# Performance work log

Measured on AMD Instinct MI355X. Metric: run time of the kernel, lower is better.

Reference implementation:

```python
import jax, jax.numpy as jnp
import numpy as np

WEIGHT = 1.0  # init kwarg
B, N, M, D = 32, 128, 128, 256


def _hungarian(cost):
    """O(n^3) Hungarian (Jonker-Volgenant potentials form) on host numpy.
    cost: [n, m] with n <= m. Returns col index assigned to each row
    (row_ind is implicitly arange(n), matching scipy.linear_sum_assignment).
    """
    cost = np.asarray(cost, dtype=np.float64)
    n, m = cost.shape
    u = np.zeros(n + 1)
    v = np.zeros(m + 1)
    p = np.zeros(m + 1, dtype=np.int64)   # p[j] = row (1-based) matched to col j
    way = np.zeros(m + 1, dtype=np.int64)
    for i in range(1, n + 1):
        p[0] = i
        j0 = 0
        minv = np.full(m + 1, np.inf)
        used = np.zeros(m + 1, dtype=bool)
        while True:
            used[j0] = True
            i0 = p[j0]
            free = ~used[1:]
            cur = cost[i0 - 1, :] - u[i0] - v[1:]
            upd = free & (cur < minv[1:])
            minv[1:][upd] = cur[upd]
            way[1:][upd] = j0
            masked = np.where(free, minv[1:], np.inf)
            j1 = int(np.argmin(masked)) + 1
            delta = masked[j1 - 1]
            u[p[used]] += delta
            v[used] -= delta
            minv[1:][free] -= delta
            j0 = j1
            if p[j0] == 0:
                break
        while j0:
            j1 = way[j0]
            p[j0] = p[j1]
            j0 = j1
    col_of_row = np.zeros(n, dtype=np.int64)
    for j in range(1, m + 1):
        if p[j] > 0:
            col_of_row[p[j] - 1] = j - 1
    return col_of_row


def _pairwise_mse(p, g):
    """cost[b,i,j] = mean_d (p[b,i,d]-g[b,j,d])^2, fused without [B,N,M,D] tensor."""
    d = p.shape[-1]
    p2 = jnp.sum(p * p, axis=-1)                    # [B,N]
    g2 = jnp.sum(g * g, axis=-1)                    # [B,M]
    pg = jnp.einsum('bnd,bmd->bnm', p, g)           # [B,N,M]
    return (p2[:, :, None] + g2[:, None, :] - 2.0 * pg) / d


def setup_inputs() -> dict:
    key = jax.random.key(0)
    k1, k2 = jax.random.split(key)
    batch_prediction = jax.random.normal(k1, (B, N, D), dtype=jnp.float32)
    batch_groundtruth = jax.random.normal(k2, (B, M, D), dtype=jnp.float32)
    return {"batch_prediction": batch_prediction,
            "batch_groundtruth": batch_groundtruth}


def reference(batch_prediction, batch_groundtruth):
    b, n = batch_prediction.shape[0], batch_prediction.shape[1]
    cost = _pairwise_mse(batch_prediction, batch_groundtruth)   # [B,N,M]
    cost_np = np.asarray(jax.device_get(cost))
    # Hungarian assignment on host (matches scipy.linear_sum_assignment; CPU-bound)
    cols = jnp.asarray(np.stack([_hungarian(cost_np[bi]) for bi in range(b)]))  # [B,N]
    matched = cost[jnp.arange(b)[:, None], jnp.arange(n)[None, :], cols]        # [B,N]
    loss = matched.mean(axis=1).sum() / b * WEIGHT
    return jnp.reshape(loss, (1,))
```

## Files before the change

### kernel.cpp

```cpp
#include <hip/hip_runtime.h>
#include <hip/hip_fp16.h>
#include <float.h>

#define Bc 32
#define Nn 128
#define Dd 256

#define QSCALE 2048.0f
#define QINV   (1.0f / 2048.0f)
#define GPAD   260

template <int CTRL>
__device__ __forceinline__ float dpp_addsrc(float x) {
    return __int_as_float(__builtin_amdgcn_update_dpp(0, __float_as_int(x), CTRL,
                                                      0xf, 0xf, false));
}
__device__ __forceinline__ float wave_sum_lane63(float x) {
    x += dpp_addsrc<0x121>(x);
    x += dpp_addsrc<0x122>(x);
    x += dpp_addsrc<0x124>(x);
    x += dpp_addsrc<0x128>(x);
    x += dpp_addsrc<0x142>(x);
    x += dpp_addsrc<0x143>(x);
    return x;
}

template <int CTRL>
__device__ __forceinline__ unsigned dpp_movu(unsigned x) {
    return (unsigned)__builtin_amdgcn_update_dpp((int)0xFFFFFFFFu, (int)x, CTRL,
                                                 0xf, 0xf, false);
}
__device__ __forceinline__ unsigned wave_umin_lane63(unsigned x) {
    x = min(x, dpp_movu<0x121>(x));
    x = min(x, dpp_movu<0x122>(x));
    x = min(x, dpp_movu<0x124>(x));
    x = min(x, dpp_movu<0x128>(x));
    x = min(x, dpp_movu<0x142>(x));
    x = min(x, dpp_movu<0x143>(x));
    return x;
}

template <int CTRL>
__device__ __forceinline__ float dpp_movf(float x) {
    return __int_as_float(__builtin_amdgcn_update_dpp(0x7f7fffff, __float_as_int(x),
                                                      CTRL, 0xf, 0xf, false));
}
template <int CTRL>
__device__ __forceinline__ void dpp2min_step(float& m1, float& m2) {
    float o1 = dpp_movf<CTRL>(m1);
    float o2 = dpp_movf<CTRL>(m2);
    float n1 = fminf(m1, o1);
    m2 = fminf(fmaxf(m1, o1), fminf(m2, o2));
    m1 = n1;
}

__device__ __forceinline__ float readlane_f(float v, int lane) {
    return __int_as_float(__builtin_amdgcn_readlane(__float_as_int(v), lane));
}

__global__ __launch_bounds__(256) void matcher_kernel(const float* __restrict__ P,
                                                      const float* __restrict__ G,
                                                      float* __restrict__ ws,
                                                      float* __restrict__ out) {
    const int b = blockIdx.x;
    const int tid = threadIdx.x;
    const int t = tid & 63;
    const int wv = tid >> 6;

    __shared__ float Csh[Nn * Nn];
    __shared__ float gsh[64 * GPAD];
    __shared__ float p2sh[Nn];
    __shared__ int claim[Nn];
    __half2* H = (__half2*)gsh;

    if (tid < Nn) {
        claim[tid] = 0x7fffffff;
        const float4* pr = (const float4*)(P + ((size_t)b * Nn + tid) * Dd);
        float s = 0.f;
        for (int d4 = 0; d4 < Dd / 4; ++d4) {
            float4 v = pr[d4];
            s += v.x * v.x + v.y * v.y + v.z * v.z + v.w * v.w;
        }
        p2sh[tid] = s;
    }

    const float4* G4 = (const float4*)(G + (size_t)b * Nn * Dd);
    for (int h = 0; h < 2; ++h) {
        __syncthreads();
        for (int k = 0; k < 16; ++k) {
            int e = k * 256 + tid;
            int row = e >> 6, c4 = e & 63;
            *(float4*)&gsh[row * GPAD + c4 * 4] = G4[(size_t)(h * 64 + row) * 64 + c4];
        }
        __syncthreads();

        const int jj = t;
        float g2 = 0.f;
        for (int d4 = 0; d4 < 64; ++d4) {
            float4 gv = *(const float4*)&gsh[jj * GPAD + d4 * 4];
            g2 += gv.x * gv.x + gv.y * gv.y + gv.z * gv.z + gv.w * gv.w;
        }
        for (int ii = wv; ii < Nn; ii += 4) {
            const float4* prow = (const float4*)(P + ((size_t)b * Nn + ii) * Dd);
            float pg = 0.f;
#pragma unroll 8
            for (int d4 = 0; d4 < 64; ++d4) {
                float4 pv = prow[d4];
                float4 gv = *(const float4*)&gsh[jj * GPAD + d4 * 4];
                pg += pv.x * gv.x + pv.y * gv.y + pv.z * gv.z + pv.w * gv.w;
            }
            Csh[ii * Nn + h * 64 + jj] =
                (p2sh[ii] + g2 - 2.0f * pg) * (1.0f / (float)Dd);
        }
    }
    __syncthreads();

    for (int e = tid; e < Nn * 64; e += 256) {
        int row = e >> 6, c = e & 63;
        H[e] = __halves2half2(__float2half_rn(Csh[row * Nn + c]),
                              __float2half_rn(Csh[row * Nn + c + 64]));
    }
    __syncthreads();
    if (wv != 0) return;

    float bestA = FLT_MAX, bestB = FLT_MAX;
    int argA = 0, argB = 0;
    for (int i = 0; i < Nn; ++i) {
        __half2 hc = H[i * 64 + t];
        float c0 = __low2float(hc);
        float c1 = __high2float(hc);
        if (c0 < bestA) { bestA = c0; argA = i; }
        if (c1 < bestB) { bestB = c1; argB = i; }
    }
    float vA = bestA, vB = bestB;
    atomicMin(&claim[argA], t);
    atomicMin(&claim[argB], t + 64);

    float uA = 0.0f, uB = 0.0f;
    int pA = 0, pB = 0;
    if (claim[argA] == t)      pA = argA + 1;
    if (claim[argB] == t + 64) pB = argB + 1;

    unsigned long long fmA = __ballot(claim[t] == 0x7fffffff);
    unsigned long long fmB = __ballot(claim[t + 64] == 0x7fffffff);

    for (int pass = 0; pass < 3; ++pass) {
        if (!(fmA | fmB)) break;
        unsigned long long remA = fmA, remB = fmB;
        int guard = 0;
        while ((remA | remB) != 0ull && guard++ < 256) {
            int l, i, slotR;
            if (remA) { l = __ffsll(remA) - 1; remA &= remA - 1; i = l + 1;  slotR = 0;
                        if (!((fmA >> l) & 1)) continue; }
            else      { l = __ffsll(remB) - 1; remB &= remB - 1; i = l + 65; slotR = 1;
                        if (!((fmB >> l) & 1)) continue; }

            __half2 hr = H[(i - 1) * 64 + t];
            float cur0 = __low2float(hr) - vA;
            float cur1 = __high2float(hr) - vB;
            float m1 = fminf(cur0, cur1);
            float m2 = fmaxf(cur0, cur1);
            dpp2min_step<0x121>(m1, m2);
            dpp2min_step<0x122>(m1, m2);
            dpp2min_step<0x124>(m1, m2);
            dpp2min_step<0x128>(m1, m2);
            dpp2min_step<0x142>(m1, m2);
            dpp2min_step<0x143>(m1, m2);
            float s_m1 = readlane_f(m1, 63);
            float s_m2 = readlane_f(m2, 63);

            unsigned long long b0 = __ballot(cur0 == s_m1);
            unsigned long long b1 = __ballot(cur1 == s_m1);
            int j1 = b0 ? __ffsll(b0) : (__ffsll(b1) + 64);
            int lane1 = (j1 - 1) & 63, slot1 = (j1 - 1) >> 6;

            if (t == l) { if (slotR == 0) uA = s_m2; else uB = s_m2; }

            int k0 = __builtin_amdgcn_readlane(slot1 ? pB : pA, lane1);
            bool strict = (s_m1 < s_m2);
            if (!strict && k0 != 0) continue;

            if (t == lane1) {
                if (slot1 == 0) { vA += s_m1 - s_m2; pA = i; }
                else            { vB += s_m1 - s_m2; pB = i; }
            }
            if (slotR == 0) fmA &= ~(1ull << l); else fmB &= ~(1ull << l);
            if (k0 != 0) {
                int kl = (k0 - 1) & 63;
                if (k0 <= 64) { fmA |= 1ull << kl; remA |= 1ull << kl; }
                else          { fmB |= 1ull << kl; remB |= 1ull << kl; }
            }
        }
    }

    for (int slotR = 0; slotR < 2; ++slotR) {
        unsigned long long mask = slotR ? fmB : fmA;
        while (mask) {
            int l = __ffsll(mask) - 1;
            mask &= mask - 1;
            int i = l + 1 + slotR * 64;

            float minvA = FLT_MAX, minvB = FLT_MAX;
            int wayA = -1, wayB = -1;
            bool usedA = false, usedB = false;
            bool rUA = false, rUB = false;
            if (t == l) { if (slotR == 0) rUA = true; else rUB = true; }

            int s_j0 = -1;
            float s_u = readlane_f(slotR ? uB : uA, l);
            int s_j1;

            __half2 hc = H[(i - 1) * 64 + t];

            for (;;) {
                float c0 = __low2float(hc);
                float c1 = __high2float(hc);
                if (!usedA) {
                    float cur = fmaxf(c0 - s_u - vA, 0.0f);
                    if (cur < minvA) { minvA = cur; wayA = s_j0; }
                }
                if (!usedB) {
                    float cur = fmaxf(c1 - s_u - vB, 0.0f);
                    if (cur < minvB) { minvB = cur; wayB = s_j0; }
                }

                unsigned kA = usedA ? 0xFFFFFFFFu
                    : ((((unsigned)(fminf(minvA, 30.0f) * QSCALE)) << 16)
                       | ((unsigned)pA << 8) | (unsigned)t);
                unsigned kB = usedB ? 0xFFFFFFFFu
                    : ((((unsigned)(fminf(minvB, 30.0f) * QSCALE)) << 16)
                       | ((unsigned)pB << 8) | (unsigned)(t + 64));
                unsigned k = wave_umin_lane63(min(kA, kB));
                unsigned s_key = (unsigned)__builtin_amdgcn_readlane((int)k, 63);
                float s_delta = (float)(s_key >> 16) * QINV;
                int s_p = (int)((s_key >> 8) & 0xFFu);
                s_j1 = (int)(s_key & 0xFFu);

                int idx = (s_p > 0 ? s_p : 1) - 1;
                __half2 nhc = H[idx * 64 + t];
                float s_unext = readlane_f((idx >> 6) ? uB : uA, idx & 63);

                if (usedA) { vA -= s_delta; } else { minvA = fmaxf(minvA - s_delta, 0.0f); }
                if (usedB) { vB -= s_delta; } else { minvB = fmaxf(minvB - s_delta, 0.0f); }
                if (rUA) uA += s_delta;
                if (rUB) uB += s_delta;

                if (s_p == 0) break;

                if (t == (s_j1 & 63)) { if ((s_j1 >> 6) == 0) usedA = true; else usedB = true; }
                {
                    int r = s_p - 1;
                    if (t == (r & 63)) { if ((r >> 6) == 0) rUA = true; else rUB = true; }
                }
                s_j0 = s_j1;
                s_u = s_unext;
                hc = nhc;
            }

            int s_j = s_j1;
            while (s_j >= 0) {
                int lane = s_j & 63;
                int slot = s_j >> 6;
                int s_jprev = __builtin_amdgcn_readlane(slot ? wayB : wayA, lane);
                int s_pnew;
                if (s_jprev < 0) {
                    s_pnew = i;
                } else {
                    int lp = s_jprev & 63;
                    int sp = s_jprev >> 6;
                    s_pnew = __builtin_amdgcn_readlane(sp ? pB : pA, lp);
                }
                if (t == lane) {
                    if (slot == 0) pA = s_pnew; else pB = s_pnew;
                }
                s_j = s_jprev;
            }
        }
    }

    float tot = Csh[(pA - 1) * Nn + t] + Csh[(pB - 1) * Nn + t + 64];
    tot = wave_sum_lane63(tot);

    if (t == 63) {
        __hip_atomic_store(&ws[b], tot, __ATOMIC_RELEASE, __HIP_MEMORY_SCOPE_AGENT);
    }

    if (b == 0) {
        float v = 0.f;
        if (t < Bc) {
            do {
                v = __hip_atomic_load(&ws[t], __ATOMIC_ACQUIRE, __HIP_MEMORY_SCOPE_AGENT);
            } while (!(v > 0.0f));
        }
        float x = (t < Bc) ? v : 0.0f;
        x = wave_sum_lane63(x);
        if (t == 63) out[0] = x * (1.0f / ((float)Nn * (float)Bc));
    }
}

extern "C" void kernel_launch(void* const* d_in, const int* in_sizes, int n_in,
                              void* d_out, int out_size, void* d_ws, size_t ws_size,
                              hipStream_t stream) {
    const float* P = (const float*)d_in[0];
    const float* G = (const float*)d_in[1];
    float* out = (float*)d_out;
    float* ws = (float*)d_ws;

    matcher_kernel<<<Bc, 256, 0, stream>>>(P, G, ws, out);
}
```

Measured before the change: 581.9 us.

## Use fp32 cost matrix and lazy dual updates in Hungarian augmentation

Drops the fp16 half2 copy of the cost matrix and reads fp32 costs straight from shared memory. The Dijkstra-style augmentation now keeps absolute distances and applies the potential updates once after each search, instead of updating every lane's minv, u and v on each iteration. This takes per-step ALU work out of the serial single-wave loop. The p2/g2/pg dot products are split into four independent accumulators to expose more ILP. Risks are twice the LDS traffic per row fetch and a change in numerics, since quantized keys are now built from absolute distances clamped at 30.

```diff
diff --git a/kernel.cpp b/kernel.cpp
--- a/kernel.cpp
+++ b/kernel.cpp
@@ -1,5 +1,4 @@
 #include <hip/hip_runtime.h>
-#include <hip/hip_fp16.h>
 #include <float.h>
 
 #define Bc 32
@@ -7,7 +6,6 @@
 #define Dd 256
 
 #define QSCALE 2048.0f
-#define QINV   (1.0f / 2048.0f)
 #define GPAD   260
 
 template <int CTRL>
@@ -58,6 +56,10 @@
     return __int_as_float(__builtin_amdgcn_readlane(__float_as_int(v), lane));
 }
 
+__device__ __forceinline__ float dot4(float4 a, float4 b) {
+    return a.x * b.x + a.y * b.y + a.z * b.z + a.w * b.w;
+}
+
 __global__ __launch_bounds__(256) void matcher_kernel(const float* __restrict__ P,
                                                       const float* __restrict__ G,
                                                       float* __restrict__ ws,
@@ -71,17 +73,20 @@
     __shared__ float gsh[64 * GPAD];
     __shared__ float p2sh[Nn];
     __shared__ int claim[Nn];
-    __half2* H = (__half2*)gsh;
 
     if (tid < Nn) {
         claim[tid] = 0x7fffffff;
         const float4* pr = (const float4*)(P + ((size_t)b * Nn + tid) * Dd);
-        float s = 0.f;
-        for (int d4 = 0; d4 < Dd / 4; ++d4) {
-            float4 v = pr[d4];
-            s += v.x * v.x + v.y * v.y + v.z * v.z + v.w * v.w;
-        }
-        p2sh[tid] = s;
+        float a0 = 0.f, a1 = 0.f, a2 = 0.f, a3 = 0.f;
+#pragma unroll
+        for (int d4 = 0; d4 < 64; d4 += 4) {
+            float4 v0 = pr[d4], v1 = pr[d4 + 1], v2 = pr[d4 + 2], v3 = pr[d4 + 3];
+            a0 += dot4(v0, v0);
+            a1 += dot4(v1, v1);
+            a2 += dot4(v2, v2);
+            a3 += dot4(v3, v3);
+        }
+        p2sh[tid] = (a0 + a1) + (a2 + a3);
     }
 
     const float4* G4 = (const float4*)(G + (size_t)b * Nn * Dd);
@@ -95,30 +100,42 @@
         __syncthreads();
 
         const int jj = t;
-        float g2 = 0.f;
-        for (int d4 = 0; d4 < 64; ++d4) {
-            float4 gv = *(const float4*)&gsh[jj * GPAD + d4 * 4];
-            g2 += gv.x * gv.x + gv.y * gv.y + gv.z * gv.z + gv.w * gv.w;
+        float g2;
+        {
+            float a0 = 0.f, a1 = 0.f, a2 = 0.f, a3 = 0.f;
+#pragma unroll
+            for (int d4 = 0; d4 < 64; d4 += 4) {
+                float4 v0 = *(const float4*)&gsh[jj * GPAD + d4 * 4];
+                float4 v1 = *(const float4*)&gsh[jj * GPAD + (d4 + 1) * 4];
+                float4 v2 = *(const float4*)&gsh[jj * GPAD + (d4 + 2) * 4];
+                float4 v3 = *(const float4*)&gsh[jj * GPAD + (d4 + 3) * 4];
+                a0 += dot4(v0, v0);
+                a1 += dot4(v1, v1);
+                a2 += dot4(v2, v2);
+                a3 += dot4(v3, v3);
+            }
+            g2 = (a0 + a1) + (a2 + a3);
         }
         for (int ii = wv; ii < Nn; ii += 4) {
             const float4* prow = (const float4*)(P + ((size_t)b * Nn + ii) * Dd);
-            float pg = 0.f;
-#pragma unroll 8
-            for (int d4 = 0; d4 < 64; ++d4) {
-                float4 pv = prow[d4];
-                float4 gv = *(const float4*)&gsh[jj * GPAD + d4 * 4];
-                pg += pv.x * gv.x + pv.y * gv.y + pv.z * gv.z + pv.w * gv.w;
-            }
+            float a0 = 0.f, a1 = 0.f, a2 = 0.f, a3 = 0.f;
+#pragma unroll
+            for (int d4 = 0; d4 < 64; d4 += 4) {
+                float4 p0 = prow[d4], p1 = prow[d4 + 1];
+                float4 p2 = prow[d4 + 2], p3 = prow[d4 + 3];
+                float4 q0 = *(const float4*)&gsh[jj * GPAD + d4 * 4];
+                float4 q1 = *(const float4*)&gsh[jj * GPAD + (d4 + 1) * 4];
+                float4 q2 = *(const float4*)&gsh[jj * GPAD + (d4 + 2) * 4];
+                float4 q3 = *(const float4*)&gsh[jj * GPAD + (d4 + 3) * 4];
+                a0 += dot4(p0, q0);
+                a1 += dot4(p1, q1);
+                a2 += dot4(p2, q2);
+                a3 += dot4(p3, q3);
+            }
+            float pg = (a0 + a1) + (a2 + a3);
             Csh[ii * Nn + h * 64 + jj] =
                 (p2sh[ii] + g2 - 2.0f * pg) * (1.0f / (float)Dd);
         }
-    }
-    __syncthreads();
-
-    for (int e = tid; e < Nn * 64; e += 256) {
-        int row = e >> 6, c = e & 63;
-        H[e] = __halves2half2(__float2half_rn(Csh[row * Nn + c]),
-                              __float2half_rn(Csh[row * Nn + c + 64]));
     }
     __syncthreads();
     if (wv != 0) return;
@@ -126,9 +143,8 @@
     float bestA = FLT_MAX, bestB = FLT_MAX;
     int argA = 0, argB = 0;
     for (int i = 0; i < Nn; ++i) {
-        __half2 hc = H[i * 64 + t];
-        float c0 = __low2float(hc);
-        float c1 = __high2float(hc);
+        float c0 = Csh[i * Nn + t];
+        float c1 = Csh[i * Nn + t + 64];
         if (c0 < bestA) { bestA = c0; argA = i; }
         if (c1 < bestB) { bestB = c1; argB = i; }
     }
@@ -155,9 +171,9 @@
             else      { l = __ffsll(remB) - 1; remB &= remB - 1; i = l + 65; slotR = 1;
                         if (!((fmB >> l) & 1)) continue; }
 
-            __half2 hr = H[(i - 1) * 64 + t];
-            float cur0 = __low2float(hr) - vA;
-            float cur1 = __high2float(hr) - vB;
+            const float* crow = &Csh[(i - 1) * Nn];
+            float cur0 = crow[t] - vA;
+            float cur1 = crow[t + 64] - vB;
             float m1 = fminf(cur0, cur1);
             float m2 = fmaxf(cur0, cur1);
             dpp2min_step<0x121>(m1, m2);
@@ -200,62 +216,66 @@
             mask &= mask - 1;
             int i = l + 1 + slotR * 64;
 
-            float minvA = FLT_MAX, minvB = FLT_MAX;
+            float dA = FLT_MAX, dB = FLT_MAX;
             int wayA = -1, wayB = -1;
             bool usedA = false, usedB = false;
-            bool rUA = false, rUB = false;
-            if (t == l) { if (slotR == 0) rUA = true; else rUB = true; }
 
             int s_j0 = -1;
+            float s_mu = 0.0f;
             float s_u = readlane_f(slotR ? uB : uA, l);
             int s_j1;
 
-            __half2 hc = H[(i - 1) * 64 + t];
+            float c0 = Csh[(i - 1) * Nn + t];
+            float c1 = Csh[(i - 1) * Nn + t + 64];
 
             for (;;) {
-                float c0 = __low2float(hc);
-                float c1 = __high2float(hc);
+                float s_base = s_mu - s_u;
                 if (!usedA) {
-                    float cur = fmaxf(c0 - s_u - vA, 0.0f);
-                    if (cur < minvA) { minvA = cur; wayA = s_j0; }
+                    float cur = fmaxf(c0 - vA + s_base, 0.0f);
+                    if (cur < dA) { dA = cur; wayA = s_j0; }
                 }
                 if (!usedB) {
-                    float cur = fmaxf(c1 - s_u - vB, 0.0f);
-                    if (cur < minvB) { minvB = cur; wayB = s_j0; }
+                    float cur = fmaxf(c1 - vB + s_base, 0.0f);
+                    if (cur < dB) { dB = cur; wayB = s_j0; }
                 }
 
                 unsigned kA = usedA ? 0xFFFFFFFFu
-                    : ((((unsigned)(fminf(minvA, 30.0f) * QSCALE)) << 16)
+                    : ((((unsigned)(fminf(dA, 30.0f) * QSCALE)) << 16)
                        | ((unsigned)pA << 8) | (unsigned)t);
                 unsigned kB = usedB ? 0xFFFFFFFFu
-                    : ((((unsigned)(fminf(minvB, 30.0f) * QSCALE)) << 16)
+                    : ((((unsigned)(fminf(dB, 30.0f) * QSCALE)) << 16)
                        | ((unsigned)pB << 8) | (unsigned)(t + 64));
                 unsigned k = wave_umin_lane63(min(kA, kB));
                 unsigned s_key = (unsigned)__builtin_amdgcn_readlane((int)k, 63);
-                float s_delta = (float)(s_key >> 16) * QINV;
                 int s_p = (int)((s_key >> 8) & 0xFFu);
                 s_j1 = (int)(s_key & 0xFFu);
 
                 int idx = (s_p > 0 ? s_p : 1) - 1;
-                __half2 nhc = H[idx * 64 + t];
+                float nc0 = Csh[idx * Nn + t];
+                float nc1 = Csh[idx * Nn + t + 64];
                 float s_unext = readlane_f((idx >> 6) ? uB : uA, idx & 63);
-
-                if (usedA) { vA -= s_delta; } else { minvA = fmaxf(minvA - s_delta, 0.0f); }
-                if (usedB) { vB -= s_delta; } else { minvB = fmaxf(minvB - s_delta, 0.0f); }
-                if (rUA) uA += s_delta;
-                if (rUB) uB += s_delta;
+                s_mu = readlane_f((s_j1 >> 6) ? dB : dA, s_j1 & 63);
 
                 if (s_p == 0) break;
 
                 if (t == (s_j1 & 63)) { if ((s_j1 >> 6) == 0) usedA = true; else usedB = true; }
-                {
-                    int r = s_p - 1;
-                    if (t == (r & 63)) { if ((r >> 6) == 0) rUA = true; else rUB = true; }
-                }
                 s_j0 = s_j1;
                 s_u = s_unext;
-                hc = nhc;
-            }
+                c0 = nc0;
+                c1 = nc1;
+            }
+
+            float mustar = s_mu;
+            {
+                int r = i - 1;
+                if (t == (r & 63)) { if ((r >> 6) == 0) uA += mustar; else uB += mustar; }
+            }
+            p2sh[t] = 0.0f;
+            p2sh[t + 64] = 0.0f;
+            if (usedA) { float adj = mustar - dA; vA -= adj; p2sh[pA - 1] = adj; }
+            if (usedB) { float adj = mustar - dB; vB -= adj; p2sh[pB - 1] = adj; }
+            uA += p2sh[t];
+            uB += p2sh[t + 64];
 
             int s_j = s_j1;
             while (s_j >= 0) {
```

Measured after the change: 723.8 us. 24.4% more time.

## Use fp32 cost matrix directly and double block to 512 threads

Applied to the files above, without the earlier changes.

Removes the fp16 half2 packed copy of the cost matrix and has the single-wave Hungarian solver read fp32 costs straight from shared memory. The pairwise-MSE phase is spread over 512 threads (8 waves) instead of 256. This drops one conversion pass and a barrier, and avoids fp16 rounding in the assignment. In exchange, each solver step now does two LDS loads per lane instead of one, and those loads sit on the serial critical path.

```diff
diff --git a/kernel.cpp b/kernel.cpp
--- a/kernel.cpp
+++ b/kernel.cpp
@@ -1,5 +1,4 @@
 #include <hip/hip_runtime.h>
-#include <hip/hip_fp16.h>
 #include <float.h>
 
 #define Bc 32
@@ -58,7 +57,7 @@
     return __int_as_float(__builtin_amdgcn_readlane(__float_as_int(v), lane));
 }
 
-__global__ __launch_bounds__(256) void matcher_kernel(const float* __restrict__ P,
+__global__ __launch_bounds__(512) void matcher_kernel(const float* __restrict__ P,
                                                       const float* __restrict__ G,
                                                       float* __restrict__ ws,
                                                       float* __restrict__ out) {
@@ -71,7 +70,6 @@
     __shared__ float gsh[64 * GPAD];
     __shared__ float p2sh[Nn];
     __shared__ int claim[Nn];
-    __half2* H = (__half2*)gsh;
 
     if (tid < Nn) {
         claim[tid] = 0x7fffffff;
@@ -87,8 +85,8 @@
     const float4* G4 = (const float4*)(G + (size_t)b * Nn * Dd);
     for (int h = 0; h < 2; ++h) {
         __syncthreads();
-        for (int k = 0; k < 16; ++k) {
-            int e = k * 256 + tid;
+        for (int k = 0; k < 8; ++k) {
+            int e = k * 512 + tid;
             int row = e >> 6, c4 = e & 63;
             *(float4*)&gsh[row * GPAD + c4 * 4] = G4[(size_t)(h * 64 + row) * 64 + c4];
         }
@@ -100,7 +98,7 @@
             float4 gv = *(const float4*)&gsh[jj * GPAD + d4 * 4];
             g2 += gv.x * gv.x + gv.y * gv.y + gv.z * gv.z + gv.w * gv.w;
         }
-        for (int ii = wv; ii < Nn; ii += 4) {
+        for (int ii = wv; ii < Nn; ii += 8) {
             const float4* prow = (const float4*)(P + ((size_t)b * Nn + ii) * Dd);
             float pg = 0.f;
 #pragma unroll 8
@@ -114,21 +112,13 @@
         }
     }
     __syncthreads();
-
-    for (int e = tid; e < Nn * 64; e += 256) {
-        int row = e >> 6, c = e & 63;
-        H[e] = __halves2half2(__float2half_rn(Csh[row * Nn + c]),
-                              __float2half_rn(Csh[row * Nn + c + 64]));
-    }
-    __syncthreads();
     if (wv != 0) return;
 
     float bestA = FLT_MAX, bestB = FLT_MAX;
     int argA = 0, argB = 0;
     for (int i = 0; i < Nn; ++i) {
-        __half2 hc = H[i * 64 + t];
-        float c0 = __low2float(hc);
-        float c1 = __high2float(hc);
+        float c0 = Csh[i * Nn + t];
+        float c1 = Csh[i * Nn + t + 64];
         if (c0 < bestA) { bestA = c0; argA = i; }
         if (c1 < bestB) { bestB = c1; argB = i; }
     }
@@ -155,9 +145,9 @@
             else      { l = __ffsll(remB) - 1; remB &= remB - 1; i = l + 65; slotR = 1;
                         if (!((fmB >> l) & 1)) continue; }
 
-            __half2 hr = H[(i - 1) * 64 + t];
-            float cur0 = __low2float(hr) - vA;
-            float cur1 = __high2float(hr) - vB;
+            const float* crow = &Csh[(i - 1) * Nn];
+            float cur0 = crow[t] - vA;
+            float cur1 = crow[t + 64] - vB;
             float m1 = fminf(cur0, cur1);
             float m2 = fmaxf(cur0, cur1);
             dpp2min_step<0x121>(m1, m2);
@@ -210,11 +200,10 @@
             float s_u = readlane_f(slotR ? uB : uA, l);
             int s_j1;
 
-            __half2 hc = H[(i - 1) * 64 + t];
+            float c0 = Csh[(i - 1) * Nn + t];
+            float c1 = Csh[(i - 1) * Nn + t + 64];
 
             for (;;) {
-                float c0 = __low2float(hc);
-                float c1 = __high2float(hc);
                 if (!usedA) {
                     float cur = fmaxf(c0 - s_u - vA, 0.0f);
                     if (cur < minvA) { minvA = cur; wayA = s_j0; }
@@ -237,7 +226,8 @@
                 s_j1 = (int)(s_key & 0xFFu);
 
                 int idx = (s_p > 0 ? s_p : 1) - 1;
-                __half2 nhc = H[idx * 64 + t];
+                float nc0 = Csh[idx * Nn + t];
+                float nc1 = Csh[idx * Nn + t + 64];
                 float s_unext = readlane_f((idx >> 6) ? uB : uA, idx & 63);
 
                 if (usedA) { vA -= s_delta; } else { minvA = fmaxf(minvA - s_delta, 0.0f); }
@@ -254,7 +244,8 @@
                 }
                 s_j0 = s_j1;
                 s_u = s_unext;
-                hc = nhc;
+                c0 = nc0;
+                c1 = nc1;
             }
 
             int s_j = s_j1;
@@ -306,5 +297,5 @@
     float* out = (float*)d_out;
     float* ws = (float*)d_ws;
 
-    matcher_kernel<<<Bc, 256, 0, stream>>>(P, G, ws, out);
-}
+    matcher_kernel<<<Bc, 512, 0, stream>>>(P, G, ws, out);
+}
```

Measured after the change: 691.4 us. +18.8%, slower.
